# Optimization experiments

Hardware: AMD Instinct MI355X
Metric: run time of the kernel (lower is better)

## Reference

```python
import jax, jax.numpy as jnp
import numpy as np

B, N, D = 2, 2048, 1024   # batch, seq_len, d_model
E = 2 * D                  # d_inner = d_model * expand_factor
F = 4 * D                  # ffn hidden
CHUNK = 128
EPS_LN = 1e-5


def setup_inputs() -> dict:
    key = jax.random.key(0)
    ks = jax.random.split(key, 16)
    s = 0.02
    return {
        "x": jax.random.normal(ks[0], (B, N, D), dtype=jnp.float32),
        # linear-attention projections (stored [in, out])
        "q_w": jax.random.normal(ks[1], (D, E), dtype=jnp.float32) * s,
        "q_b": jnp.zeros((E,), jnp.float32),
        "k_w": jax.random.normal(ks[2], (D, E), dtype=jnp.float32) * s,
        "k_b": jnp.zeros((E,), jnp.float32),
        "v_w": jax.random.normal(ks[3], (D, E), dtype=jnp.float32) * s,
        "v_b": jnp.zeros((E,), jnp.float32),
        "o_w": jax.random.normal(ks[4], (E, D), dtype=jnp.float32) * s,
        "o_b": jnp.zeros((D,), jnp.float32),
        # layer norms
        "ln1_g": jnp.ones((D,), jnp.float32), "ln1_b": jnp.zeros((D,), jnp.float32),
        "ln2_g": jnp.ones((D,), jnp.float32), "ln2_b": jnp.zeros((D,), jnp.float32),
        # ffn
        "w1": jax.random.normal(ks[5], (D, F), dtype=jnp.float32) * s,
        "b1": jnp.zeros((F,), jnp.float32),
        "w2": jax.random.normal(ks[6], (F, D), dtype=jnp.float32) * s,
        "b2": jnp.zeros((D,), jnp.float32),
    }


def _layer_norm(x, g, b):
    mu = jnp.mean(x, axis=-1, keepdims=True)
    var = jnp.mean(jnp.square(x - mu), axis=-1, keepdims=True)
    return (x - mu) * jax.lax.rsqrt(var + EPS_LN) * g + b


def _feature_map(x):
    return jax.nn.elu(x) + 1.0  # positive features


def _causal_linear_attention(Q, K, V):
    """Exactly cumsum(k v^T) formulation, computed chunk-recurrently.
    Q,K: [B,N,E] (post feature map), V: [B,N,E]. Returns [B,N,E]."""
    nC = N // CHUNK
    Qc = Q.reshape(B, nC, CHUNK, E).transpose(1, 0, 2, 3)
    Kc = K.reshape(B, nC, CHUNK, E).transpose(1, 0, 2, 3)
    Vc = V.reshape(B, nC, CHUNK, E).transpose(1, 0, 2, 3)
    tril = jnp.tril(jnp.ones((CHUNK, CHUNK), Q.dtype))

    def step(S, qkv):  # S: [B,E,E] running sum of k v^T
        q, k, v = qkv
        scores = jnp.einsum('bcd,bkd->bck', q, k) * tril  # intra-chunk causal
        intra = jnp.einsum('bck,bke->bce', scores, v)
        inter = jnp.einsum('bcd,bde->bce', q, S)
        S = S + jnp.einsum('bcd,bce->bde', k, v)
        return S, intra + inter

    S0 = jnp.zeros((B, E, E), Q.dtype)
    _, num = jax.lax.scan(step, S0, (Qc, Kc, Vc))  # [nC,B,CHUNK,E]
    num = num.transpose(1, 0, 2, 3).reshape(B, N, E)
    Z = jnp.cumsum(K, axis=1)                       # [B,N,E]
    den = jnp.einsum('bnd,bnd->bn', Q, Z)[..., None] + 1e-6
    return num / den


def reference(x, q_w, q_b, k_w, k_b, v_w, v_b, o_w, o_b,
              ln1_g, ln1_b, ln2_g, ln2_b, w1, b1, w2, b2):
    # training branch of SSDFLUIDLayer (linear attention), dropout = identity (eval)
    xn = _layer_norm(x, ln1_g, ln1_b)
    Q = _feature_map(xn @ q_w + q_b)
    K = _feature_map(xn @ k_w + k_b)
    V = xn @ v_w + v_b
    attn = _causal_linear_attention(Q, K, V) @ o_w + o_b
    x = x + attn
    xn2 = _layer_norm(x, ln2_g, ln2_b)
    ffn = jax.nn.gelu(xn2 @ w1 + b1, approximate=False) @ w2 + b2
    return x + ffn
```

## Files before the change

### kernel.cpp

```cpp
#include <hip/hip_runtime.h>
#include <math.h>

typedef unsigned short u16;
typedef short s16x8 __attribute__((ext_vector_type(8)));
typedef float f32x4 __attribute__((ext_vector_type(4)));
typedef long long ll;

__device__ inline u16 f2bf(float f) {
    unsigned u = __float_as_uint(f);
    u += 0x7fffu + ((u >> 16) & 1u);
    return (u16)(u >> 16);
}
__device__ inline float bf2f(u16 h) { return __uint_as_float(((unsigned)h) << 16); }

__device__ __forceinline__ void glds16(const u16* g, u16* l) {
    __builtin_amdgcn_global_load_lds(
        (__attribute__((address_space(1))) void*)(void*)g,
        (__attribute__((address_space(3))) void*)l, 16, 0, 0);
}

__global__ __launch_bounds__(256) void ln_bf16(const float* __restrict__ x,
                                               const float* __restrict__ g,
                                               const float* __restrict__ b,
                                               u16* __restrict__ out, int D) {
    int row = blockIdx.x;
    const float* xr = x + (size_t)row * D;
    int t = threadIdx.x;
    float4 v = ((const float4*)xr)[t];
    float s = v.x + v.y + v.z + v.w;
    __shared__ float sm[4];
    #pragma unroll
    for (int o = 32; o > 0; o >>= 1) s += __shfl_down(s, o, 64);
    int lane = t & 63, wv = t >> 6;
    if (lane == 0) sm[wv] = s;
    __syncthreads();
    float mean = (sm[0] + sm[1] + sm[2] + sm[3]) * (1.0f / 1024.0f);
    float dx = v.x - mean, dy = v.y - mean, dz = v.z - mean, dw = v.w - mean;
    float s2 = dx * dx + dy * dy + dz * dz + dw * dw;
    __syncthreads();
    #pragma unroll
    for (int o = 32; o > 0; o >>= 1) s2 += __shfl_down(s2, o, 64);
    if (lane == 0) sm[wv] = s2;
    __syncthreads();
    float var = (sm[0] + sm[1] + sm[2] + sm[3]) * (1.0f / 1024.0f);
    float rstd = rsqrtf(var + 1e-5f);
    float4 gg = ((const float4*)g)[t], bb = ((const float4*)b)[t];
    ushort4 o4;
    o4.x = f2bf(dx * rstd * gg.x + bb.x);
    o4.y = f2bf(dy * rstd * gg.y + bb.y);
    o4.z = f2bf(dz * rstd * gg.z + bb.z);
    o4.w = f2bf(dw * rstd * gg.w + bb.w);
    ((ushort4*)(out + (size_t)row * D))[t] = o4;
}

__global__ __launch_bounds__(256) void combine_ln(
    const float* __restrict__ x, const float* __restrict__ p0,
    const float* __restrict__ p1, const float* __restrict__ ob,
    const float* __restrict__ g, const float* __restrict__ b,
    float* __restrict__ x2, u16* __restrict__ xn2) {
    int row = blockIdx.x;
    int t = threadIdx.x;
    size_t base = (size_t)row * 256;
    float4 v = ((const float4*)x)[base + t];
    float4 a0 = ((const float4*)p0)[base + t];
    float4 a1 = ((const float4*)p1)[base + t];
    float4 ob4 = ((const float4*)ob)[t];
    v.x += a0.x + a1.x + ob4.x;
    v.y += a0.y + a1.y + ob4.y;
    v.z += a0.z + a1.z + ob4.z;
    v.w += a0.w + a1.w + ob4.w;
    ((float4*)x2)[base + t] = v;
    float s = v.x + v.y + v.z + v.w;
    __shared__ float sm[4];
    #pragma unroll
    for (int o = 32; o > 0; o >>= 1) s += __shfl_down(s, o, 64);
    int lane = t & 63, wv = t >> 6;
    if (lane == 0) sm[wv] = s;
    __syncthreads();
    float mean = (sm[0] + sm[1] + sm[2] + sm[3]) * (1.0f / 1024.0f);
    float dx = v.x - mean, dy = v.y - mean, dz = v.z - mean, dw = v.w - mean;
    float s2 = dx * dx + dy * dy + dz * dz + dw * dw;
    __syncthreads();
    #pragma unroll
    for (int o = 32; o > 0; o >>= 1) s2 += __shfl_down(s2, o, 64);
    if (lane == 0) sm[wv] = s2;
    __syncthreads();
    float var = (sm[0] + sm[1] + sm[2] + sm[3]) * (1.0f / 1024.0f);
    float rstd = rsqrtf(var + 1e-5f);
    float4 gg = ((const float4*)g)[t], bb = ((const float4*)b)[t];
    ushort4 o4;
    o4.x = f2bf(dx * rstd * gg.x + bb.x);
    o4.y = f2bf(dy * rstd * gg.y + bb.y);
    o4.z = f2bf(dz * rstd * gg.z + bb.z);
    o4.w = f2bf(dw * rstd * gg.w + bb.w);
    ((ushort4*)(xn2 + (size_t)row * 1024))[t] = o4;
}

__global__ __launch_bounds__(256) void combine_out(
    const float* __restrict__ x2, const float* __restrict__ p0,
    const float* __restrict__ p1, const float* __restrict__ b2,
    float* __restrict__ out) {
    size_t i = (size_t)blockIdx.x * 256 + threadIdx.x;
    int col4 = (int)(i & 255);
    float4 v = ((const float4*)x2)[i];
    float4 a0 = ((const float4*)p0)[i];
    float4 a1 = ((const float4*)p1)[i];
    float4 bb = ((const float4*)b2)[col4];
    v.x += a0.x + a1.x + bb.x;
    v.y += a0.y + a1.y + bb.y;
    v.z += a0.z + a1.z + bb.z;
    v.w += a0.w + a1.w + bb.w;
    ((float4*)out)[i] = v;
}

__global__ void prep(const float* __restrict__ qb, const float* __restrict__ kb,
                     const float* __restrict__ vb, float* __restrict__ bcat,
                     float* __restrict__ den, int E, int BN) {
    int i = blockIdx.x * 256 + threadIdx.x;
    if (i < E) {
        bcat[i] = qb[i];
        bcat[E + i] = kb[i];
        bcat[2 * E + i] = vb[i];
    }
    if (i < BN) den[i] = 0.f;
}

__global__ __launch_bounds__(256) void transpose_all(
    const float* __restrict__ q_w, const float* __restrict__ k_w,
    const float* __restrict__ v_w, const float* __restrict__ o_w,
    const float* __restrict__ w1, const float* __restrict__ w2,
    u16* __restrict__ qkvT, u16* __restrict__ oT,
    u16* __restrict__ w1T, u16* __restrict__ w2T) {
    int z = blockIdx.y;
    const float* src;
    u16* dst;
    int R, C, tprLog;
    switch (z) {
        case 0: src = q_w; dst = qkvT;                           R = 1024; C = 2048; tprLog = 6; break;
        case 1: src = k_w; dst = qkvT + (size_t)2 * 1024 * 1024; R = 1024; C = 2048; tprLog = 6; break;
        case 2: src = v_w; dst = qkvT + (size_t)4 * 1024 * 1024; R = 1024; C = 2048; tprLog = 6; break;
        case 3: src = o_w; dst = oT;                             R = 2048; C = 1024; tprLog = 5; break;
        case 4: src = w1;  dst = w1T;                            R = 1024; C = 4096; tprLog = 7; break;
        default: src = w2; dst = w2T;                            R = 4096; C = 1024; tprLog = 5; break;
    }
    int bx = blockIdx.x;
    int ntiles = (R >> 5) << (tprLog);
    if (bx >= ntiles) return;
    int c0 = (bx & ((1 << tprLog) - 1)) * 32;
    int r0 = (bx >> tprLog) * 32;
    __shared__ u16 tile[32][33];
    int tx = threadIdx.x & 31, ty = threadIdx.x >> 5;
    #pragma unroll
    for (int i = 0; i < 32; i += 8)
        tile[ty + i][tx] = f2bf(src[(size_t)(r0 + ty + i) * C + c0 + tx]);
    __syncthreads();
    #pragma unroll
    for (int i = 0; i < 32; i += 8)
        dst[(size_t)(c0 + ty + i) * R + r0 + tx] = tile[tx][ty + i];
}

__global__ __launch_bounds__(256) void transpose_u16(const u16* __restrict__ in,
                                                     u16* __restrict__ out,
                                                     int R, int C, int ldIn,
                                                     ll sIn, ll sOut) {
    in += (size_t)blockIdx.z * sIn;
    out += (size_t)blockIdx.z * sOut;
    __shared__ u16 tile[32][33];
    int tx = threadIdx.x & 31, ty = threadIdx.x >> 5;
    int c0 = blockIdx.x * 32, r0 = blockIdx.y * 32;
    #pragma unroll
    for (int i = 0; i < 32; i += 8)
        tile[ty + i][tx] = in[(size_t)(r0 + ty + i) * ldIn + c0 + tx];
    __syncthreads();
    #pragma unroll
    for (int i = 0; i < 32; i += 8)
        out[(size_t)(c0 + ty + i) * R + r0 + tx] = tile[tx][ty + i];
}

enum { EPI_QKV = 0, EPI_TRIL = 2, EPI_DIV = 3, EPI_GELU = 5, EPI_PART = 6 };

#define TM 128
#define TN 128

template <int EPI, int BKt>
__global__ __launch_bounds__(256) void gemm_nt(
    const u16* __restrict__ A, const u16* __restrict__ B, void* __restrict__ Cv,
    const float* __restrict__ bias, float* __restrict__ den,
    int M, int N, int K, int lda, int ldb,
    ll sA, ll sB, ll sC, ll sAux) {
    int z = blockIdx.z;
    A += (size_t)z * sA;
    B += (size_t)z * sB;

    int p = blockIdx.y * gridDim.x + blockIdx.x;
    int m0, n0;
    if (EPI == EPI_TRIL || EPI == EPI_DIV) {
        int nb = gridDim.x;
        int panel = nb * 4;
        int pp = p / panel, rr = p - pp * panel;
        m0 = (pp * 4 + (rr & 3)) * TM;
        n0 = (rr >> 2) * TN;
    } else {
        int g = p & 7, r = p >> 3;
        int lw = gridDim.x >> 2, lh = gridDim.y >> 1;
        int ly = r / lw, lx = r - ly * lw;
        m0 = ((g >> 2) * lh + ly) * TM;
        n0 = ((g & 3) * lw + lx) * TN;
    }

    int t = threadIdx.x;

    if (EPI == EPI_TRIL && n0 > m0 + (TM - 1)) {
        u16* C = (u16*)Cv + (size_t)z * sC;
        #pragma unroll
        for (int s = 0; s < 8; ++s) {
            int v = t + 256 * s;
            int row = v >> 4, cf = (v & 15) * 8;
            *(uint4*)&C[(size_t)(m0 + row) * N + n0 + cf] = make_uint4(0, 0, 0, 0);
        }
        return;
    }

    __shared__ __align__(16) u16 As[TM * BKt];
    __shared__ __align__(16) u16 Bs[TN * BKt];

    f32x4 acc[4][4];
    #pragma unroll
    for (int i = 0; i < 4; i++)
        #pragma unroll
        for (int j = 0; j < 4; j++) { f32x4 zz = {0.f, 0.f, 0.f, 0.f}; acc[i][j] = zz; }

    int kend = (EPI == EPI_DIV) ? (m0 + TM < K ? m0 + TM : K) : K;

    int lane = t & 63, wv = t >> 6;
    int lr = lane & 15, q = lane >> 4;
    int wm = (wv & 1) * 64, wn = (wv >> 1) * 64;

    u16* lA = As + wv * 32 * BKt;
    u16* lB = Bs + wv * 32 * BKt;

    int srow, skf;
    if (BKt == 32) {
        srow = wv * 32 + (lane >> 2);
        skf = (((lane & 3) - ((lane >> 3) & 3)) & 3) * 8;
    } else {
        srow = wv * 32 + (lane >> 3);
        skf = (((lane & 7) - (lane >> 3)) & 7) * 8;
    }
    const u16* gA0 = A + (size_t)(m0 + srow) * lda + skf;
    const u16* gB0 = B + (size_t)(n0 + srow) * ldb + skf;

    int ca[2][4], cb[2][4];
    #pragma unroll
    for (int i = 0; i < 4; i++) {
        int ra = wm + i * 16 + lr;
        int rb = wn + i * 16 + lr;
        if (BKt == 32) {
            ca[0][i] = (ra * 4 + ((q + (ra >> 1)) & 3)) * 8;
            cb[0][i] = (rb * 4 + ((q + (rb >> 1)) & 3)) * 8;
        } else {
            ca[0][i] = (ra * 8 + ((q + (ra & 7)) & 7)) * 8;
            ca[1][i] = (ra * 8 + ((4 + q + (ra & 7)) & 7)) * 8;
            cb[0][i] = (rb * 8 + ((q + (rb & 7)) & 7)) * 8;
            cb[1][i] = (rb * 8 + ((4 + q + (rb & 7)) & 7)) * 8;
        }
    }

    for (int k0 = 0; k0 < kend; k0 += BKt) {
        if (BKt == 32) {
            glds16(gA0 + k0, lA);
            glds16(gA0 + k0 + (size_t)16 * lda, lA + 16 * BKt);
            glds16(gB0 + k0, lB);
            glds16(gB0 + k0 + (size_t)16 * ldb, lB + 16 * BKt);
        } else {
            #pragma unroll
            for (int r = 0; r < 4; ++r) {
                glds16(gA0 + k0 + (size_t)(8 * r) * lda, lA + r * 8 * BKt);
                glds16(gB0 + k0 + (size_t)(8 * r) * ldb, lB + r * 8 * BKt);
            }
        }
        __syncthreads();
        #pragma unroll
        for (int kk = 0; kk < BKt / 32; ++kk) {
            s16x8 af[4], bfr[4];
            #pragma unroll
            for (int i = 0; i < 4; i++) af[i] = *(const s16x8*)&As[ca[kk][i]];
            #pragma unroll
            for (int j = 0; j < 4; j++) bfr[j] = *(const s16x8*)&Bs[cb[kk][j]];
            #pragma unroll
            for (int i = 0; i < 4; i++)
                #pragma unroll
                for (int j = 0; j < 4; j++)
                    acc[i][j] = __builtin_amdgcn_mfma_f32_16x16x32_bf16(af[i], bfr[j], acc[i][j], 0, 0, 0);
        }
        __syncthreads();
    }

    u16* Cb = (u16*)Cv + (size_t)z * sC;
    float* Cf = (float*)Cv + (size_t)z * sC;
    bool isQK = (EPI == EPI_QKV) && (n0 < 4096);
    #pragma unroll
    for (int i = 0; i < 4; i++) {
        #pragma unroll
        for (int r = 0; r < 4; r++) {
            int row = m0 + wm + i * 16 + q * 4 + r;
            float rs = 0.f;
            #pragma unroll
            for (int j = 0; j < 4; j++) {
                int col = n0 + wn + j * 16 + lr;
                float v = acc[i][j][r];
                if (EPI == EPI_QKV) {
                    v += bias[col];
                    if (isQK) v = (v > 0.f) ? (v + 1.f) : __expf(v);
                    Cb[(size_t)row * N + col] = f2bf(v);
                } else if (EPI == EPI_TRIL) {
                    v = (col <= row) ? v : 0.f;
                    rs += v;
                    Cb[(size_t)row * N + col] = f2bf(v);
                } else if (EPI == EPI_DIV) {
                    float d = den[(size_t)z * sAux + row] + 1e-6f;
                    Cb[(size_t)row * N + col] = f2bf(v / d);
                } else if (EPI == EPI_GELU) {
                    v += bias[col];
                    float u = v * (0.7978845608f + 0.0356774081f * v * v);
                    u = fminf(u, 40.f);
                    float e = __expf(2.f * u);
                    v = v * __fdividef(e, e + 1.f);
                    Cb[(size_t)row * N + col] = f2bf(v);
                } else if (EPI == EPI_PART) {
                    Cf[(size_t)row * N + col] = v;
                }
            }
            if (EPI == EPI_TRIL) {
                #pragma unroll
                for (int m = 1; m < 16; m <<= 1) rs += __shfl_xor(rs, m, 16);
                if (lr == 0) atomicAdd(&den[(size_t)z * sAux + row], rs);
            }
        }
    }
}

extern "C" void kernel_launch(void* const* d_in, const int* in_sizes, int n_in,
                              void* d_out, int out_size, void* d_ws, size_t ws_size,
                              hipStream_t stream) {
    const float* x    = (const float*)d_in[0];
    const float* q_w  = (const float*)d_in[1];
    const float* q_b  = (const float*)d_in[2];
    const float* k_w  = (const float*)d_in[3];
    const float* k_b  = (const float*)d_in[4];
    const float* v_w  = (const float*)d_in[5];
    const float* v_b  = (const float*)d_in[6];
    const float* o_w  = (const float*)d_in[7];
    const float* o_b  = (const float*)d_in[8];
    const float* ln1g = (const float*)d_in[9];
    const float* ln1b = (const float*)d_in[10];
    const float* ln2g = (const float*)d_in[11];
    const float* ln2b = (const float*)d_in[12];
    const float* w1   = (const float*)d_in[13];
    const float* b1   = (const float*)d_in[14];
    const float* w2   = (const float*)d_in[15];
    const float* b2   = (const float*)d_in[16];
    float* out = (float*)d_out;

    constexpr int Bb = 2, N = 2048, D = 1024, E = 2048, F = 4096;
    constexpr int BN = Bb * N;
    constexpr int E3 = 3 * E;

    char* ws = (char*)d_ws;
    size_t off = 0;
    auto alloc = [&](size_t bytes) -> void* {
        void* p = ws + off;
        off += (bytes + 255) & ~(size_t)255;
        return p;
    };
    u16*   qkvT = (u16*)alloc((size_t)E3 * D * 2);
    u16*   oT   = (u16*)alloc((size_t)D * E * 2);
    u16*   w1T  = (u16*)alloc((size_t)F * D * 2);
    u16*   w2T  = (u16*)alloc((size_t)D * F * 2);
    float* bcat = (float*)alloc((size_t)E3 * 4);
    u16*   xn   = (u16*)alloc((size_t)BN * D * 2);
    u16*   QKV  = (u16*)alloc((size_t)BN * E3 * 2);
    u16*   Vt   = (u16*)alloc((size_t)Bb * E * N * 2);
    u16*   Amat = (u16*)alloc((size_t)Bb * N * N * 2);
    float* den  = (float*)alloc((size_t)BN * 4);

    u16*   xn2 = xn;
    u16*   P   = QKV;
    u16*   h   = QKV + (size_t)8 * 1024 * 1024;
    float* x2  = (float*)Vt;
    float* pt0 = (float*)Amat;
    float* pt1 = pt0 + (size_t)BN * D;

    dim3 blk(256);

    prep<<<dim3((BN + 255) / 256), blk, 0, stream>>>(q_b, k_b, v_b, bcat, den, E, BN);

    transpose_all<<<dim3(4096, 6), blk, 0, stream>>>(
        q_w, k_w, v_w, o_w, w1, w2, qkvT, oT, w1T, w2T);

    ln_bf16<<<BN, blk, 0, stream>>>(x, ln1g, ln1b, xn, D);

    gemm_nt<EPI_QKV, 64><<<dim3(E3 / 128, BN / 128, 1), blk, 0, stream>>>(
        xn, qkvT, QKV, bcat, nullptr, BN, E3, D, D, D, 0, 0, 0, 0);

    transpose_u16<<<dim3(E / 32, N / 32, Bb), blk, 0, stream>>>(
        QKV + 2 * E, Vt, N, E, E3, (ll)N * E3, (ll)E * N);

    gemm_nt<EPI_TRIL, 64><<<dim3(N / 128, N / 128, Bb), blk, 0, stream>>>(
        QKV, QKV + E, Amat, nullptr, den, N, N, E, E3, E3,
        (ll)N * E3, (ll)N * E3, (ll)N * N, (ll)N);

    gemm_nt<EPI_DIV, 64><<<dim3(E / 128, N / 128, Bb), blk, 0, stream>>>(
        Amat, Vt, P, nullptr, den, N, E, N, N, N,
        (ll)N * N, (ll)E * N, (ll)N * E, (ll)N);

    gemm_nt<EPI_PART, 64><<<dim3(D / 128, BN / 128, 2), blk, 0, stream>>>(
        P, oT, pt0, nullptr, nullptr, BN, D, E / 2, E, E,
        (ll)(E / 2), (ll)(E / 2), (ll)BN * D, 0);

    combine_ln<<<BN, blk, 0, stream>>>(x, pt0, pt1, o_b, ln2g, ln2b, x2, xn2);

    gemm_nt<EPI_GELU, 64><<<dim3(F / 128, BN / 128, 1), blk, 0, stream>>>(
        xn2, w1T, h, b1, nullptr, BN, F, D, D, D, 0, 0, 0, 0);

    gemm_nt<EPI_PART, 64><<<dim3(D / 128, BN / 128, 2), blk, 0, stream>>>(
        h, w2T, pt0, nullptr, nullptr, BN, D, F / 2, F, F,
        (ll)(F / 2), (ll)(F / 2), (ll)BN * D, 0);

    combine_out<<<dim3(BN * D / 4 / 256), blk, 0, stream>>>(x2, pt0, pt1, b2, out);
}
```

Before: 465.3 us.

## Add 256x256-tile 8-wave GEMM with interleaved staging for QKV and FFN1

```diff
diff --git a/kernel.cpp b/kernel.cpp
--- a/kernel.cpp
+++ b/kernel.cpp
@@ -340,6 +340,168 @@
     }
 }
 
+template <int EPI>
+__global__ __launch_bounds__(512, 2) void gemm_nt256(
+    const u16* __restrict__ A, const u16* __restrict__ B, u16* __restrict__ C,
+    const float* __restrict__ bias, int M, int N, int K, int lda, int ldb) {
+
+    __shared__ __align__(16) u16 lds[2][4][128 * 64];
+
+    int p = blockIdx.y * gridDim.x + blockIdx.x;
+    int g = p & 7, rr = p >> 3;
+    int lw = gridDim.x >> 2, lh = gridDim.y >> 1;
+    int ly = rr / lw, lx = rr - ly * lw;
+    int m0 = ((g >> 2) * lh + ly) * 256;
+    int n0 = ((g & 3) * lw + lx) * 256;
+
+    int t = threadIdx.x;
+    int lane = t & 63, wid = t >> 6;
+    int lr = lane & 15, q = lane >> 4;
+
+    int sr = wid * 16 + (lane >> 3);
+    int skf = (((lane & 7) - (lane >> 3)) & 7) * 8;
+    const u16* gA = A + (size_t)(m0 + sr) * lda + skf;
+    const u16* gB = B + (size_t)(n0 + sr) * ldb + skf;
+    int sd = wid * 1024;
+
+    int nk = K >> 6;
+
+    auto stage = [&](int half, int tt, int d) {
+        int kt = tt < nk ? tt : nk - 1;
+        const u16* s = (half < 2 ? gA + (size_t)(half * 128) * lda
+                                 : gB + (size_t)((half - 2) * 128) * ldb) + kt * 64;
+        size_t ld = (half < 2) ? (size_t)lda : (size_t)ldb;
+        glds16(s, &lds[d][half][sd]);
+        glds16(s + 8 * ld, &lds[d][half][sd + 512]);
+    };
+
+    f32x4 acc[8][4];
+    #pragma unroll
+    for (int i = 0; i < 8; i++)
+        #pragma unroll
+        for (int j = 0; j < 4; j++) { f32x4 zz = {0.f, 0.f, 0.f, 0.f}; acc[i][j] = zz; }
+
+    int ha = wid >> 2;
+    int hb = (wid >> 1) & 1;
+    int vb0 = lr * 64 + (((q + lr) & 7) << 3);
+    int vb1 = lr * 64 + (((4 + q + lr) & 7) << 3);
+    int bb = (wid & 1) * 4096;
+
+    stage(0, 0, 0); stage(1, 0, 0); stage(2, 0, 0); stage(3, 0, 0);
+    stage(2, 1, 1); stage(0, 1, 1);
+    asm volatile("s_waitcnt vmcnt(4)" ::: "memory");
+    asm volatile("s_barrier" ::: "memory");
+
+    s16x8 a[4][2], b0[2][2], b1[2][2];
+
+    for (int tt = 0; tt < nk; ++tt) {
+        int cur = tt & 1, nxt = cur ^ 1;
+        const u16* Ah = &lds[cur][ha][0];
+        const u16* Bh = &lds[cur][2 + hb][bb];
+
+        #pragma unroll
+        for (int i = 0; i < 4; i++) {
+            a[i][0] = *(const s16x8*)&Ah[vb0 + i * 1024];
+            a[i][1] = *(const s16x8*)&Ah[vb1 + i * 1024];
+        }
+        #pragma unroll
+        for (int j = 0; j < 2; j++) {
+            b0[j][0] = *(const s16x8*)&Bh[vb0 + j * 1024];
+            b0[j][1] = *(const s16x8*)&Bh[vb1 + j * 1024];
+        }
+        stage(1, tt + 1, nxt);
+        asm volatile("s_barrier" ::: "memory");
+        asm volatile("s_waitcnt lgkmcnt(0)" ::: "memory");
+        __builtin_amdgcn_s_setprio(1);
+        #pragma unroll
+        for (int i = 0; i < 4; i++)
+            #pragma unroll
+            for (int j = 0; j < 2; j++) {
+                acc[i][j] = __builtin_amdgcn_mfma_f32_16x16x32_bf16(a[i][0], b0[j][0], acc[i][j], 0, 0, 0);
+                acc[i][j] = __builtin_amdgcn_mfma_f32_16x16x32_bf16(a[i][1], b0[j][1], acc[i][j], 0, 0, 0);
+            }
+        __builtin_amdgcn_s_setprio(0);
+        asm volatile("s_barrier" ::: "memory");
+
+        #pragma unroll
+        for (int j = 0; j < 2; j++) {
+            b1[j][0] = *(const s16x8*)&Bh[2048 + vb0 + j * 1024];
+            b1[j][1] = *(const s16x8*)&Bh[2048 + vb1 + j * 1024];
+        }
+        stage(3, tt + 1, nxt);
+        asm volatile("s_barrier" ::: "memory");
+        asm volatile("s_waitcnt lgkmcnt(0)" ::: "memory");
+        __builtin_amdgcn_s_setprio(1);
+        #pragma unroll
+        for (int i = 0; i < 4; i++)
+            #pragma unroll
+            for (int j = 0; j < 2; j++) {
+                acc[i][2 + j] = __builtin_amdgcn_mfma_f32_16x16x32_bf16(a[i][0], b1[j][0], acc[i][2 + j], 0, 0, 0);
+                acc[i][2 + j] = __builtin_amdgcn_mfma_f32_16x16x32_bf16(a[i][1], b1[j][1], acc[i][2 + j], 0, 0, 0);
+            }
+        __builtin_amdgcn_s_setprio(0);
+        asm volatile("s_barrier" ::: "memory");
+
+        #pragma unroll
+        for (int i = 0; i < 4; i++) {
+            a[i][0] = *(const s16x8*)&Ah[4096 + vb0 + i * 1024];
+            a[i][1] = *(const s16x8*)&Ah[4096 + vb1 + i * 1024];
+        }
+        stage(2, tt + 2, cur);
+        asm volatile("s_barrier" ::: "memory");
+        asm volatile("s_waitcnt lgkmcnt(0)" ::: "memory");
+        __builtin_amdgcn_s_setprio(1);
+        #pragma unroll
+        for (int i = 0; i < 4; i++)
+            #pragma unroll
+            for (int j = 0; j < 2; j++) {
+                acc[4 + i][2 + j] = __builtin_amdgcn_mfma_f32_16x16x32_bf16(a[i][0], b1[j][0], acc[4 + i][2 + j], 0, 0, 0);
+                acc[4 + i][2 + j] = __builtin_amdgcn_mfma_f32_16x16x32_bf16(a[i][1], b1[j][1], acc[4 + i][2 + j], 0, 0, 0);
+            }
+        __builtin_amdgcn_s_setprio(0);
+        asm volatile("s_barrier" ::: "memory");
+
+        stage(0, tt + 2, cur);
+        asm volatile("s_barrier" ::: "memory");
+        __builtin_amdgcn_s_setprio(1);
+        #pragma unroll
+        for (int i = 0; i < 4; i++)
+            #pragma unroll
+            for (int j = 0; j < 2; j++) {
+                acc[4 + i][j] = __builtin_amdgcn_mfma_f32_16x16x32_bf16(a[i][0], b0[j][0], acc[4 + i][j], 0, 0, 0);
+                acc[4 + i][j] = __builtin_amdgcn_mfma_f32_16x16x32_bf16(a[i][1], b0[j][1], acc[4 + i][j], 0, 0, 0);
+            }
+        __builtin_amdgcn_s_setprio(0);
+        asm volatile("s_waitcnt vmcnt(4)" ::: "memory");
+        asm volatile("s_barrier" ::: "memory");
+    }
+
+    asm volatile("s_waitcnt vmcnt(0)" ::: "memory");
+
+    int wm = (wid >> 2) * 128, wn = (wid & 3) * 64;
+    #pragma unroll
+    for (int mi = 0; mi < 8; mi++) {
+        #pragma unroll
+        for (int r = 0; r < 4; r++) {
+            int row = m0 + wm + mi * 16 + q * 4 + r;
+            #pragma unroll
+            for (int nj = 0; nj < 4; nj++) {
+                int col = n0 + wn + nj * 16 + lr;
+                float v = acc[mi][nj][r] + bias[col];
+                if (EPI == EPI_QKV) {
+                    if (n0 + wn + nj * 16 < 4096) v = (v > 0.f) ? (v + 1.f) : __expf(v);
+                } else {
+                    float u = v * (0.7978845608f + 0.0356774081f * v * v);
+                    u = fminf(u, 40.f);
+                    float e = __expf(2.f * u);
+                    v = v * __fdividef(e, e + 1.f);
+                }
+                C[(size_t)row * N + col] = f2bf(v);
+            }
+        }
+    }
+}
+
 extern "C" void kernel_launch(void* const* d_in, const int* in_sizes, int n_in,
                               void* d_out, int out_size, void* d_ws, size_t ws_size,
                               hipStream_t stream) {
@@ -400,8 +562,8 @@
 
     ln_bf16<<<BN, blk, 0, stream>>>(x, ln1g, ln1b, xn, D);
 
-    gemm_nt<EPI_QKV, 64><<<dim3(E3 / 128, BN / 128, 1), blk, 0, stream>>>(
-        xn, qkvT, QKV, bcat, nullptr, BN, E3, D, D, D, 0, 0, 0, 0);
+    gemm_nt256<EPI_QKV><<<dim3(E3 / 256, BN / 256), dim3(512), 0, stream>>>(
+        xn, qkvT, QKV, bcat, BN, E3, D, D, D);
 
     transpose_u16<<<dim3(E / 32, N / 32, Bb), blk, 0, stream>>>(
         QKV + 2 * E, Vt, N, E, E3, (ll)N * E3, (ll)E * N);
@@ -420,8 +582,8 @@
 
     combine_ln<<<BN, blk, 0, stream>>>(x, pt0, pt1, o_b, ln2g, ln2b, x2, xn2);
 
-    gemm_nt<EPI_GELU, 64><<<dim3(F / 128, BN / 128, 1), blk, 0, stream>>>(
-        xn2, w1T, h, b1, nullptr, BN, F, D, D, D, 0, 0, 0, 0);
+    gemm_nt256<EPI_GELU><<<dim3(F / 256, BN / 256), dim3(512), 0, stream>>>(
+        xn2, w1T, h, b1, BN, F, D, D, D);
 
     gemm_nt<EPI_PART, 64><<<dim3(D / 128, BN / 128, 2), blk, 0, stream>>>(
         h, w2T, pt0, nullptr, nullptr, BN, D, F / 2, F, F,
```

New measurement: 458.5 us. No clear change (-1.5%).

## Add triple-buffered 128x256 GEMM kernel for QKV and FFN-up projections

Applied to the files above, without the earlier changes.

```diff
diff --git a/kernel.cpp b/kernel.cpp
--- a/kernel.cpp
+++ b/kernel.cpp
@@ -340,6 +340,138 @@
     }
 }
 
+template <int EPI>
+__global__ __launch_bounds__(512, 2) void gemm3b(
+    const u16* __restrict__ A, const u16* __restrict__ B, u16* __restrict__ C,
+    const float* __restrict__ bias, int M, int N, int K, int lda, int ldb) {
+
+    __shared__ __align__(16) u16 lds[3][24576];
+
+    int p = blockIdx.y * gridDim.x + blockIdx.x;
+    int g = p & 7, rr = p >> 3;
+    int lw = gridDim.x >> 2, lh = gridDim.y >> 1;
+    int ly = rr / lw, lx = rr - ly * lw;
+    int m0 = ((g >> 2) * lh + ly) * 128;
+    int n0 = ((g & 3) * lw + lx) * 256;
+
+    int t = threadIdx.x;
+    int lane = t & 63, wid = t >> 6;
+    int lr = lane & 15, q = lane >> 4;
+
+    int skf = (((lane & 7) - (lane >> 3)) & 7) * 8;
+    const u16* gA = A + (size_t)(m0 + wid * 16 + (lane >> 3)) * lda + skf;
+    const u16* gB = B + (size_t)(n0 + wid * 32 + (lane >> 3)) * ldb + skf;
+    int sdA = wid * 1024;
+    int sdB = 8192 + wid * 2048;
+
+    int nk = K >> 6;
+
+    auto stageA = [&](int tt, int d) {
+        int kt = (tt < nk ? tt : nk - 1) << 6;
+        glds16(gA + kt, &lds[d][sdA]);
+        glds16(gA + kt + (size_t)8 * lda, &lds[d][sdA + 512]);
+    };
+    auto stageB = [&](int tt, int d) {
+        int kt = (tt < nk ? tt : nk - 1) << 6;
+        #pragma unroll
+        for (int r2 = 0; r2 < 4; ++r2)
+            glds16(gB + kt + (size_t)(8 * r2) * ldb, &lds[d][sdB + r2 * 512]);
+    };
+
+    f32x4 acc[4][4];
+    #pragma unroll
+    for (int i = 0; i < 4; i++)
+        #pragma unroll
+        for (int j = 0; j < 4; j++) { f32x4 zz = {0.f, 0.f, 0.f, 0.f}; acc[i][j] = zz; }
+
+    int wm = (wid >> 2) * 64, wn = (wid & 3) * 64;
+    int aoff0 = wm * 64 + lr * 64 + (((q + lr) & 7) << 3);
+    int aoff1 = wm * 64 + lr * 64 + (((4 + q + lr) & 7) << 3);
+    int boff0 = 8192 + wn * 64 + lr * 64 + (((q + lr) & 7) << 3);
+    int boff1 = 8192 + wn * 64 + lr * 64 + (((4 + q + lr) & 7) << 3);
+
+    stageA(0, 0); stageB(0, 0);
+    stageA(1, 1); stageB(1, 1);
+    asm volatile("s_waitcnt vmcnt(6)" ::: "memory");
+    asm volatile("s_barrier" ::: "memory");
+
+    s16x8 a[4][2], b[4][2];
+
+    int cur = 0;
+    for (int tt = 0; tt < nk; ++tt) {
+        int nx2 = cur + 2; if (nx2 >= 3) nx2 -= 3;
+        const u16* L = &lds[cur][0];
+
+        #pragma unroll
+        for (int j = 0; j < 2; j++) {
+            b[j][0] = *(const s16x8*)&L[boff0 + j * 1024];
+            b[j][1] = *(const s16x8*)&L[boff1 + j * 1024];
+        }
+        #pragma unroll
+        for (int i = 0; i < 4; i++) {
+            a[i][0] = *(const s16x8*)&L[aoff0 + i * 1024];
+            a[i][1] = *(const s16x8*)&L[aoff1 + i * 1024];
+        }
+        stageB(tt + 2, nx2);
+        asm volatile("s_barrier" ::: "memory");
+        __builtin_amdgcn_s_setprio(1);
+        #pragma unroll
+        for (int i = 0; i < 4; i++)
+            #pragma unroll
+            for (int j = 0; j < 2; j++) {
+                acc[i][j] = __builtin_amdgcn_mfma_f32_16x16x32_bf16(a[i][0], b[j][0], acc[i][j], 0, 0, 0);
+                acc[i][j] = __builtin_amdgcn_mfma_f32_16x16x32_bf16(a[i][1], b[j][1], acc[i][j], 0, 0, 0);
+            }
+        __builtin_amdgcn_s_setprio(0);
+        asm volatile("s_barrier" ::: "memory");
+
+        #pragma unroll
+        for (int j = 2; j < 4; j++) {
+            b[j][0] = *(const s16x8*)&L[boff0 + j * 1024];
+            b[j][1] = *(const s16x8*)&L[boff1 + j * 1024];
+        }
+        stageA(tt + 2, nx2);
+        asm volatile("s_barrier" ::: "memory");
+        __builtin_amdgcn_s_setprio(1);
+        #pragma unroll
+        for (int i = 0; i < 4; i++)
+            #pragma unroll
+            for (int j = 2; j < 4; j++) {
+                acc[i][j] = __builtin_amdgcn_mfma_f32_16x16x32_bf16(a[i][0], b[j][0], acc[i][j], 0, 0, 0);
+                acc[i][j] = __builtin_amdgcn_mfma_f32_16x16x32_bf16(a[i][1], b[j][1], acc[i][j], 0, 0, 0);
+            }
+        __builtin_amdgcn_s_setprio(0);
+        asm volatile("s_waitcnt vmcnt(6)" ::: "memory");
+        asm volatile("s_barrier" ::: "memory");
+
+        cur = cur + 1; if (cur >= 3) cur -= 3;
+    }
+
+    asm volatile("s_waitcnt vmcnt(0)" ::: "memory");
+
+    #pragma unroll
+    for (int i = 0; i < 4; i++) {
+        #pragma unroll
+        for (int r = 0; r < 4; r++) {
+            int row = m0 + wm + i * 16 + q * 4 + r;
+            #pragma unroll
+            for (int j = 0; j < 4; j++) {
+                int col = n0 + wn + j * 16 + lr;
+                float v = acc[i][j][r] + bias[col];
+                if (EPI == EPI_QKV) {
+                    if (n0 + wn + j * 16 < 4096) v = (v > 0.f) ? (v + 1.f) : __expf(v);
+                } else {
+                    float u = v * (0.7978845608f + 0.0356774081f * v * v);
+                    u = fminf(u, 40.f);
+                    float e = __expf(2.f * u);
+                    v = v * __fdividef(e, e + 1.f);
+                }
+                C[(size_t)row * N + col] = f2bf(v);
+            }
+        }
+    }
+}
+
 extern "C" void kernel_launch(void* const* d_in, const int* in_sizes, int n_in,
                               void* d_out, int out_size, void* d_ws, size_t ws_size,
                               hipStream_t stream) {
@@ -400,8 +532,8 @@
 
     ln_bf16<<<BN, blk, 0, stream>>>(x, ln1g, ln1b, xn, D);
 
-    gemm_nt<EPI_QKV, 64><<<dim3(E3 / 128, BN / 128, 1), blk, 0, stream>>>(
-        xn, qkvT, QKV, bcat, nullptr, BN, E3, D, D, D, 0, 0, 0, 0);
+    gemm3b<EPI_QKV><<<dim3(E3 / 256, BN / 128), dim3(512), 0, stream>>>(
+        xn, qkvT, QKV, bcat, BN, E3, D, D, D);
 
     transpose_u16<<<dim3(E / 32, N / 32, Bb), blk, 0, stream>>>(
         QKV + 2 * E, Vt, N, E, E3, (ll)N * E3, (ll)E * N);
@@ -420,8 +552,8 @@
 
     combine_ln<<<BN, blk, 0, stream>>>(x, pt0, pt1, o_b, ln2g, ln2b, x2, xn2);
 
-    gemm_nt<EPI_GELU, 64><<<dim3(F / 128, BN / 128, 1), blk, 0, stream>>>(
-        xn2, w1T, h, b1, nullptr, BN, F, D, D, D, 0, 0, 0, 0);
+    gemm3b<EPI_GELU><<<dim3(F / 256, BN / 128), dim3(512), 0, stream>>>(
+        xn2, w1T, h, b1, BN, F, D, D, D);
 
     gemm_nt<EPI_PART, 64><<<dim3(D / 128, BN / 128, 2), blk, 0, stream>>>(
         h, w2T, pt0, nullptr, nullptr, BN, D, F / 2, F, F,
```

New measurement: 459.7 us. About the same (-1.2%).
